# Optimization experiments

Measured on AMD Instinct MI355X. Metric: run time of the kernel, lower is better.

The kernel has to match this reference:

```python
import jax, jax.numpy as jnp
import numpy as np

B, S, D, H = 2, 2048, 1024, 16
DH = D // H  # dim_per_head = 64


def setup_inputs() -> dict:
    key = jax.random.key(0)
    ks = jax.random.split(key, 12)
    scale = 1.0 / np.sqrt(D)
    inp = {
        "key": jax.random.normal(ks[0], (B, S, D), jnp.float32),
        "value": jax.random.normal(ks[1], (B, S, D), jnp.float32),
        "query": jax.random.normal(ks[2], (B, S, D), jnp.float32),
        "mask": jnp.zeros((B, S, S), dtype=bool),
        # nn.Linear weights stored as [out, in]; we keep [in, out] for x @ W
        "Wk": jax.random.normal(ks[3], (D, D), jnp.float32) * scale,
        "bk": jnp.zeros((D,), jnp.float32),
        "Wv": jax.random.normal(ks[4], (D, D), jnp.float32) * scale,
        "bv": jnp.zeros((D,), jnp.float32),
        "Wq": jax.random.normal(ks[5], (D, D), jnp.float32) * scale,
        "bq": jnp.zeros((D,), jnp.float32),
        "Wo": jax.random.normal(ks[6], (D, D), jnp.float32) * scale,
        "bo": jnp.zeros((D,), jnp.float32),
    }
    return inp


def reference(key, value, query, mask, Wk, bk, Wv, bv, Wq, bq, Wo, bo):
    # project and split heads: [B, S, D] -> [B, H, S, DH]
    def shape(x):
        return x.reshape(B, S, H, DH).transpose(0, 2, 1, 3)

    k = shape(key @ Wk + bk)
    v = shape(value @ Wv + bv)
    q = shape(query @ Wq + bq) / jnp.sqrt(jnp.asarray(DH, key.dtype))

    # scores: [B, H, Sq, Sk]
    scores = jnp.einsum("bhqd,bhkd->bhqk", q, k)
    scores = jnp.where(mask[:, None, :, :], jnp.asarray(-1e10, scores.dtype), scores)
    attn = jax.nn.softmax(scores, axis=-1)
    # dropout is identity in eval mode
    context = jnp.einsum("bhqk,bhkd->bhqd", attn, v)
    context = context.transpose(0, 2, 1, 3).reshape(B, S, D)
    output = context @ Wo + bo
    return output, attn
```

## Files before the change

kernel.cpp:

```cpp
#include <hip/hip_runtime.h>

#define B_  2
#define S_  2048
#define D_  1024
#define H_  16

typedef _Float16 h8 __attribute__((ext_vector_type(8)));
typedef _Float16 h4 __attribute__((ext_vector_type(4)));
typedef float f4 __attribute__((ext_vector_type(4)));

static __device__ __forceinline__ f4 mfma16(h8 a, h8 b, f4 c) {
  return __builtin_amdgcn_mfma_f32_16x16x32_f16(a, b, c, 0, 0, 0);
}

static __device__ __forceinline__ void gload16(const void* g, void* l) {
  __builtin_amdgcn_global_load_lds(
      (const __attribute__((address_space(1))) void*)g,
      (__attribute__((address_space(3))) void*)l, 16, 0, 0);
}

struct C3 { const float* in[3]; _Float16* out[3]; };
__global__ __launch_bounds__(256) void cvt3_kernel(C3 c) {
  const float* in = c.in[blockIdx.y];
  _Float16* out = c.out[blockIdx.y];
  const size_t i = ((size_t)blockIdx.x * 256 + threadIdx.x) * 8;
  float4 a = *(const float4*)(in + i);
  float4 b = *(const float4*)(in + i + 4);
  h8 v;
  v[0]=(_Float16)a.x; v[1]=(_Float16)a.y; v[2]=(_Float16)a.z; v[3]=(_Float16)a.w;
  v[4]=(_Float16)b.x; v[5]=(_Float16)b.y; v[6]=(_Float16)b.z; v[7]=(_Float16)b.w;
  *(h8*)(out + i) = v;
}

struct W4 { const float* w[4]; _Float16* wt[4]; };
__global__ __launch_bounds__(256) void wtrans4_kernel(W4 a) {
  const float* W = a.w[blockIdx.z];
  _Float16* WT = a.wt[blockIdx.z];
  __shared__ float tile[64][65];
  const int t = threadIdx.x;
  const int bi = blockIdx.x * 64;
  const int bj = blockIdx.y * 64;
  const int row = t >> 2, c0 = (t & 3) * 16;
  const float* src = W + (size_t)(bi + row) * D_ + bj + c0;
#pragma unroll
  for (int j = 0; j < 4; j++) {
    float4 v = *(const float4*)(src + j * 4);
    tile[row][c0 + j*4 + 0] = v.x; tile[row][c0 + j*4 + 1] = v.y;
    tile[row][c0 + j*4 + 2] = v.z; tile[row][c0 + j*4 + 3] = v.w;
  }
  __syncthreads();
  h8 o0, o1;
#pragma unroll
  for (int j = 0; j < 8; j++) o0[j] = (_Float16)tile[c0 + j][row];
#pragma unroll
  for (int j = 0; j < 8; j++) o1[j] = (_Float16)tile[c0 + 8 + j][row];
  _Float16* dst = WT + (size_t)(bj + row) * D_ + bi + c0;
  *(h8*)(dst)     = o0;
  *(h8*)(dst + 8) = o1;
}

__global__ __launch_bounds__(256) void maskflag_kernel(const unsigned char* __restrict__ mask,
                                                       unsigned char* __restrict__ flags) {
  __shared__ int s;
  const int t = threadIdx.x;
  const int kt = blockIdx.x, qb = blockIdx.y, b = blockIdx.z;
  if (t == 0) s = 0;
  __syncthreads();
  const unsigned char* mp = mask + ((size_t)(b * S_ + qb * 128 + (t >> 1))) * S_
                          + kt * 64 + (t & 1) * 32;
  const uint4* p = (const uint4*)mp;
  uint4 v = p[0], w = p[1];
  unsigned int o = v.x | v.y | v.z | v.w | w.x | w.y | w.z | w.w;
  if (o) s = 1;
  __syncthreads();
  if (t == 0) flags[((size_t)b * 16 + qb) * 32 + kt] = (unsigned char)s;
}

struct GArg { const _Float16* A; const _Float16* BT; const float* bias;
              void* out; float scale; int mode; };
struct G3 { GArg a[3]; };

__global__ __launch_bounds__(256, 3) void gemmp_kernel(G3 G) {
  const GArg g = G.a[blockIdx.z];
  const _Float16* __restrict__ A  = g.A;
  const _Float16* __restrict__ BT = g.BT;
  __shared__ _Float16 Ash[128 * 64];
  __shared__ _Float16 Bsh[128 * 64];
  const int t = threadIdx.x, lane = t & 63, wave = t >> 6;
  const int lrow = lane & 15, lq = lane >> 4;
  const int m0 = blockIdx.x * 128, n0 = blockIdx.y * 128;
  const int wm = wave >> 1, wn = wave & 1;
  f4 acc[4][4];
#pragma unroll
  for (int i = 0; i < 4; i++)
#pragma unroll
    for (int j = 0; j < 4; j++) acc[i][j] = f4{0.f, 0.f, 0.f, 0.f};
  float bb[4];
#pragma unroll
  for (int j = 0; j < 4; j++) bb[j] = g.bias[n0 + wn*64 + j*16 + lrow];

  const int srow = t >> 3;
  const int lch  = (t & 7) ^ (srow & 7);
  const _Float16* asrc = A  + (size_t)(m0 + srow) * D_ + lch * 8;
  const _Float16* bsrc = BT + (size_t)(n0 + srow) * D_ + lch * 8;

  for (int k0 = 0; k0 < D_; k0 += 64) {
#pragma unroll
    for (int rnd = 0; rnd < 4; rnd++)
      gload16(asrc + (size_t)(rnd * 32) * D_ + k0,
              (char*)Ash + rnd * 4096 + wave * 1024);
#pragma unroll
    for (int rnd = 0; rnd < 4; rnd++)
      gload16(bsrc + (size_t)(rnd * 32) * D_ + k0,
              (char*)Bsh + rnd * 4096 + wave * 1024);
    __syncthreads();
#pragma unroll
    for (int kf = 0; kf < 2; kf++) {
      h8 af[4], bf[4];
#pragma unroll
      for (int i = 0; i < 4; i++) {
        int rr = wm*64 + i*16 + lrow;
        int ch = (kf*4 + lq) ^ (rr & 7);
        af[i] = *(h8*)((char*)Ash + rr*128 + ch*16);
      }
#pragma unroll
      for (int j = 0; j < 4; j++) {
        int rr = wn*64 + j*16 + lrow;
        int ch = (kf*4 + lq) ^ (rr & 7);
        bf[j] = *(h8*)((char*)Bsh + rr*128 + ch*16);
      }
#pragma unroll
      for (int i = 0; i < 4; i++)
#pragma unroll
        for (int j = 0; j < 4; j++)
          acc[i][j] = mfma16(af[i], bf[j], acc[i][j]);
    }
    __syncthreads();
  }

  if (g.mode == 0) {
    _Float16* out = (_Float16*)g.out;
#pragma unroll
    for (int i = 0; i < 4; i++) {
      int m = m0 + wm*64 + i*16 + lq*4;
#pragma unroll
      for (int j = 0; j < 4; j++) {
        int n = n0 + wn*64 + j*16 + lrow;
#pragma unroll
        for (int r = 0; r < 4; r++)
          out[(size_t)(m + r) * D_ + n] = (_Float16)((acc[i][j][r] + bb[j]) * g.scale);
      }
    }
  } else if (g.mode == 1) {
    _Float16* out = (_Float16*)g.out;
#pragma unroll
    for (int i = 0; i < 4; i++) {
      int m = m0 + wm*64 + i*16 + lq*4;
      int b = m >> 11, s = m & (S_ - 1);
#pragma unroll
      for (int j = 0; j < 4; j++) {
        int n = n0 + wn*64 + j*16 + lrow;
        int hh = n >> 6, dh = n & 63;
        h4 hv;
#pragma unroll
        for (int r = 0; r < 4; r++) hv[r] = (_Float16)(acc[i][j][r] + bb[j]);
        *(h4*)(out + ((size_t)((b * H_ + hh) * 64 + dh)) * S_ + s) = hv;
      }
    }
  } else {
    float* out = (float*)g.out;
#pragma unroll
    for (int i = 0; i < 4; i++) {
      int m = m0 + wm*64 + i*16 + lq*4;
#pragma unroll
      for (int j = 0; j < 4; j++) {
        int n = n0 + wn*64 + j*16 + lrow;
#pragma unroll
        for (int r = 0; r < 4; r++)
          out[(size_t)(m + r) * D_ + n] = acc[i][j][r] + bb[j];
      }
    }
  }
}

__global__ __launch_bounds__(512, 4) void gemmz_kernel(G3 G) {
  const GArg g = G.a[blockIdx.z];
  const _Float16* __restrict__ A  = g.A;
  const _Float16* __restrict__ BT = g.BT;
  __shared__ _Float16 Ash[128 * 64];
  __shared__ _Float16 Bsh[128 * 64];
  const int t = threadIdx.x, lane = t & 63, wave = t >> 6;
  const int lrow = lane & 15, lq = lane >> 4;
  const int m0 = blockIdx.x * 128, n0 = blockIdx.y * 128;
  const int wm = wave >> 2, wn = wave & 3;
  f4 acc[4][2];
#pragma unroll
  for (int i = 0; i < 4; i++)
#pragma unroll
    for (int j = 0; j < 2; j++) acc[i][j] = f4{0.f, 0.f, 0.f, 0.f};
  float bb[2];
#pragma unroll
  for (int j = 0; j < 2; j++) bb[j] = g.bias[n0 + wn*32 + j*16 + lrow];

  const int srow = t >> 3;
  const int lch  = (t & 7) ^ (srow & 7);
  const _Float16* a0 = A  + (size_t)(m0 + srow)      * D_ + lch * 8;
  const _Float16* a1 = A  + (size_t)(m0 + 64 + srow) * D_ + lch * 8;
  const _Float16* b0 = BT + (size_t)(n0 + srow)      * D_ + lch * 8;
  const _Float16* b1 = BT + (size_t)(n0 + 64 + srow) * D_ + lch * 8;
  char* adst0 = (char*)Ash + wave * 1024;
  char* adst1 = (char*)Ash + 8192 + wave * 1024;
  char* bdst0 = (char*)Bsh + wave * 1024;
  char* bdst1 = (char*)Bsh + 8192 + wave * 1024;

  for (int k0 = 0; k0 < D_; k0 += 64) {
    gload16(a0 + k0, adst0);
    gload16(a1 + k0, adst1);
    gload16(b0 + k0, bdst0);
    gload16(b1 + k0, bdst1);
    __syncthreads();
#pragma unroll
    for (int kf = 0; kf < 2; kf++) {
      h8 af[4], bf[2];
#pragma unroll
      for (int i = 0; i < 4; i++) {
        int rr = wm*64 + i*16 + lrow;
        int ch = (kf*4 + lq) ^ (rr & 7);
        af[i] = *(h8*)((char*)Ash + rr*128 + ch*16);
      }
#pragma unroll
      for (int j = 0; j < 2; j++) {
        int rr = wn*32 + j*16 + lrow;
        int ch = (kf*4 + lq) ^ (rr & 7);
        bf[j] = *(h8*)((char*)Bsh + rr*128 + ch*16);
      }
#pragma unroll
      for (int i = 0; i < 4; i++)
#pragma unroll
        for (int j = 0; j < 2; j++)
          acc[i][j] = mfma16(af[i], bf[j], acc[i][j]);
    }
    __syncthreads();
  }

  if (g.mode == 0) {
    _Float16* out = (_Float16*)g.out;
#pragma unroll
    for (int i = 0; i < 4; i++) {
      int m = m0 + wm*64 + i*16 + lq*4;
#pragma unroll
      for (int j = 0; j < 2; j++) {
        int n = n0 + wn*32 + j*16 + lrow;
#pragma unroll
        for (int r = 0; r < 4; r++)
          out[(size_t)(m + r) * D_ + n] = (_Float16)((acc[i][j][r] + bb[j]) * g.scale);
      }
    }
  } else if (g.mode == 1) {
    _Float16* out = (_Float16*)g.out;
#pragma unroll
    for (int i = 0; i < 4; i++) {
      int m = m0 + wm*64 + i*16 + lq*4;
      int b = m >> 11, s = m & (S_ - 1);
#pragma unroll
      for (int j = 0; j < 2; j++) {
        int n = n0 + wn*32 + j*16 + lrow;
        int hh = n >> 6, dh = n & 63;
        h4 hv;
#pragma unroll
        for (int r = 0; r < 4; r++) hv[r] = (_Float16)(acc[i][j][r] + bb[j]);
        *(h4*)(out + ((size_t)((b * H_ + hh) * 64 + dh)) * S_ + s) = hv;
      }
    }
  } else {
    float* out = (float*)g.out;
#pragma unroll
    for (int i = 0; i < 4; i++) {
      int m = m0 + wm*64 + i*16 + lq*4;
#pragma unroll
      for (int j = 0; j < 2; j++) {
        int n = n0 + wn*32 + j*16 + lrow;
#pragma unroll
        for (int r = 0; r < 4; r++)
          out[(size_t)(m + r) * D_ + n] = acc[i][j][r] + bb[j];
      }
    }
  }
}

__global__ __launch_bounds__(256, 4) void attnF_kernel(
    const _Float16* __restrict__ Qp, const _Float16* __restrict__ Kp,
    const _Float16* __restrict__ VpT, const unsigned char* __restrict__ mask,
    const unsigned char* __restrict__ flags,
    float* __restrict__ attn, _Float16* __restrict__ CtxH)
{
  __shared__ char smem[40960];
  const int t = threadIdx.x, lane = t & 63, wave = t >> 6;
  const int lrow = lane & 15, lq = lane >> 4;
  const int logical = ((blockIdx.x & 7) << 7) + (blockIdx.x >> 3);
  const int bh = logical >> 5, qb = logical & 31;
  const int b = bh >> 4, h = bh & 15;
  const int q0 = qb * 64, qw = q0 + wave * 16;

  h8 qf0, qf1;
  {
    const _Float16* qp = Qp + ((size_t)(b * S_ + qw + lrow)) * D_ + h * 64 + lq * 8;
    qf0 = *(const h8*)qp;
    qf1 = *(const h8*)(qp + 32);
  }

  const int srow = t >> 3, klch = (t & 7) ^ (srow & 7);
  const _Float16* ksrc = Kp + ((size_t)(b * S_ + srow)) * D_ + h * 64 + klch * 8;
  char* kdst = smem + wave * 1024;
  const unsigned char* mflags = flags + ((size_t)(b * 16 + (qb >> 1))) * 32;
  const unsigned char* mrow0 = mask + ((size_t)(b * S_ + qw + lq*4)) * S_ + lrow;

  float lsum[4] = {0.f, 0.f, 0.f, 0.f};
  for (int kt = 0; kt < S_; kt += 256) {
#pragma unroll
    for (int rnd = 0; rnd < 8; rnd++)
      gload16(ksrc + (size_t)(kt + rnd * 32) * D_, kdst + rnd * 4096);
    __syncthreads();
#pragma unroll
    for (int c = 0; c < 16; c++) {
      int kr = c*16 + lrow, sx = kr & 7;
      h8 k0 = *(h8*)(smem + kr*128 + ((lq     ^ sx) << 4));
      h8 k1 = *(h8*)(smem + kr*128 + (((4+lq) ^ sx) << 4));
      f4 a = f4{0.f, 0.f, 0.f, 0.f};
      __builtin_amdgcn_s_setprio(1);
      a = mfma16(qf0, k0, a);
      a = mfma16(qf1, k1, a);
      __builtin_amdgcn_s_setprio(0);
      if (mflags[(kt >> 6) + (c >> 2)]) {
#pragma unroll
        for (int r = 0; r < 4; r++)
          if (mrow0[(size_t)r * S_ + kt + c*16]) a[r] = -1e10f;
      }
#pragma unroll
      for (int r = 0; r < 4; r++) lsum[r] += __expf(fminf(a[r], 75.f));
    }
    __syncthreads();
  }

  float li[4];
#pragma unroll
  for (int r = 0; r < 4; r++) {
    float cs = lsum[r];
#pragma unroll
    for (int d = 1; d < 16; d <<= 1) cs += __shfl_xor(cs, d);
    li[r] = 1.0f / cs;
  }

  char* const Vt = smem + 16384;
  char* const Pt = smem + 32768;
  const int vrow = t >> 4, vlch = (t & 15) ^ (vrow & 15);
  const _Float16* vsrc = VpT + (size_t)bh * 64 * S_ + (size_t)vrow * S_ + vlch * 8;
  char* vdst = Vt + wave * 1024;

  f4 ctx[4];
#pragma unroll
  for (int dt = 0; dt < 4; dt++) ctx[dt] = f4{0.f, 0.f, 0.f, 0.f};

  for (int kt = 0; kt < S_; kt += 128) {
#pragma unroll
    for (int rnd = 0; rnd < 4; rnd++)
      gload16(ksrc + (size_t)(kt + rnd * 32) * D_, kdst + rnd * 4096);
#pragma unroll
    for (int rnd = 0; rnd < 4; rnd++)
      gload16(vsrc + (size_t)(rnd * 16) * S_ + kt, vdst + rnd * 4096);
    __syncthreads();

#pragma unroll
    for (int hh = 0; hh < 2; hh++) {
      const int kbase = kt + hh * 64;
      const bool mf = mflags[kbase >> 6] != 0;
      const int prw = wave*16 + lq*4;
#pragma unroll
      for (int c = 0; c < 4; c++) {
        int kr = hh*64 + c*16 + lrow, sx = kr & 7;
        h8 k0 = *(h8*)(smem + kr*128 + ((lq     ^ sx) << 4));
        h8 k1 = *(h8*)(smem + kr*128 + (((4+lq) ^ sx) << 4));
        f4 a = f4{0.f, 0.f, 0.f, 0.f};
        __builtin_amdgcn_s_setprio(1);
        a = mfma16(qf0, k0, a);
        a = mfma16(qf1, k1, a);
        __builtin_amdgcn_s_setprio(0);
        if (mf) {
#pragma unroll
          for (int r = 0; r < 4; r++)
            if (mrow0[(size_t)r * S_ + kbase + c*16]) a[r] = -1e10f;
        }
        float* ap = attn + ((size_t)bh * S_ + qw + lq*4) * S_ + kbase + c*16 + lrow;
        int eb = c*32 + lrow*2;
#pragma unroll
        for (int r = 0; r < 4; r++) {
          float p = __expf(fminf(a[r], 75.f)) * li[r];
          ap[(size_t)r * S_] = p;
          int rw = prw + r;
          *(_Float16*)(Pt + rw*128 + ((((eb >> 4) ^ (rw & 7))) << 4) + (eb & 15))
              = (_Float16)p;
        }
      }
      {
        int pr2 = wave*16 + lrow, sxp = pr2 & 7;
        h8 pf0 = *(h8*)(Pt + pr2*128 + (((    lq) ^ sxp) << 4));
        h8 pf1 = *(h8*)(Pt + pr2*128 + (((4 + lq) ^ sxp) << 4));
        __builtin_amdgcn_s_setprio(1);
#pragma unroll
        for (int dt = 0; dt < 4; dt++) {
          int vr = dt*16 + lrow, sxv = vr & 15;
          h8 vf0 = *(h8*)(Vt + vr*256 + (((hh*8     + lq) ^ sxv) << 4));
          h8 vf1 = *(h8*)(Vt + vr*256 + (((hh*8 + 4 + lq) ^ sxv) << 4));
          ctx[dt] = mfma16(pf0, vf0, ctx[dt]);
          ctx[dt] = mfma16(pf1, vf1, ctx[dt]);
        }
        __builtin_amdgcn_s_setprio(0);
      }
    }
    __syncthreads();
  }

  _Float16* cp = CtxH + ((size_t)(b * S_ + qw + lq*4)) * D_ + h * 64 + lrow;
#pragma unroll
  for (int dt = 0; dt < 4; dt++)
#pragma unroll
    for (int r = 0; r < 4; r++)
      cp[(size_t)r * D_ + dt*16] = (_Float16)ctx[dt][r];
}

extern "C" void kernel_launch(void* const* d_in, const int* in_sizes, int n_in,
                              void* d_out, int out_size, void* d_ws, size_t ws_size,
                              hipStream_t stream) {
  const float* key   = (const float*)d_in[0];
  const float* value = (const float*)d_in[1];
  const float* query = (const float*)d_in[2];
  const unsigned char* mask = (const unsigned char*)d_in[3];
  const float* Wk = (const float*)d_in[4];
  const float* bk = (const float*)d_in[5];
  const float* Wv = (const float*)d_in[6];
  const float* bv = (const float*)d_in[7];
  const float* Wq = (const float*)d_in[8];
  const float* bq = (const float*)d_in[9];
  const float* Wo = (const float*)d_in[10];
  const float* bo = (const float*)d_in[11];

  char* ws = (char*)d_ws;
  _Float16* WkT  = (_Float16*)(ws + 0);
  _Float16* WvT  = (_Float16*)(ws + (size_t)2  * 1024 * 1024);
  _Float16* WqT  = (_Float16*)(ws + (size_t)4  * 1024 * 1024);
  _Float16* WoT  = (_Float16*)(ws + (size_t)6  * 1024 * 1024);
  _Float16* Qp   = (_Float16*)(ws + (size_t)8  * 1024 * 1024);
  _Float16* Kp   = (_Float16*)(ws + (size_t)16 * 1024 * 1024);
  _Float16* VpT  = (_Float16*)(ws + (size_t)24 * 1024 * 1024);
  _Float16* CtxH = (_Float16*)(ws + (size_t)32 * 1024 * 1024);
  unsigned char* flags = (unsigned char*)(ws + (size_t)40 * 1024 * 1024);

  float* outp = (float*)d_out;
  float* attn = outp + (size_t)B_ * S_ * D_;
  _Float16* qH = (_Float16*)(attn);
  _Float16* kH = (_Float16*)((char*)attn + (size_t)8  * 1024 * 1024);
  _Float16* vH = (_Float16*)((char*)attn + (size_t)16 * 1024 * 1024);

  C3 c{{query, key, value}, {qH, kH, vH}};
  cvt3_kernel<<<dim3(2048, 3), 256, 0, stream>>>(c);

  W4 w{{Wk, Wv, Wq, Wo}, {WkT, WvT, WqT, WoT}};
  wtrans4_kernel<<<dim3(16, 16, 4), 256, 0, stream>>>(w);

  maskflag_kernel<<<dim3(32, 16, 2), 256, 0, stream>>>(mask, flags);

  G3 gp{{{qH, WqT, bq, Qp, 0.125f, 0},
         {kH, WkT, bk, Kp, 1.0f,   0},
         {vH, WvT, bv, VpT, 1.0f,  1}}};
  gemmp_kernel<<<dim3(32, 8, 3), 256, 0, stream>>>(gp);

  attnF_kernel<<<1024, 256, 0, stream>>>(Qp, Kp, VpT, mask, flags, attn, CtxH);

  G3 go{{{CtxH, WoT, bo, outp, 1.0f, 2},
         {nullptr, nullptr, nullptr, nullptr, 0.f, 2},
         {nullptr, nullptr, nullptr, nullptr, 0.f, 2}}};
  gemmz_kernel<<<dim3(32, 8, 1), 512, 0, stream>>>(go);
}
```

Measured before the change: 279.0 us.

## Split softmax-denominator pass by key columns across waves with LDS reduction

In the first pass computing row sums of exp(scores), each wave now handles all 64 query rows of the block but only a quarter of each 256-key tile, instead of its own 16 rows over all keys. Each K fragment read from LDS is reused across four query groups, cutting LDS reads per MFMA. Per-wave partial sums are combined through shared memory with an extra barrier. This raises register use (four Q fragment pairs and a 4x4 accumulator array), which may hurt occupancy under launch bounds of 4 blocks.

```diff
diff --git a/kernel.cpp b/kernel.cpp
--- a/kernel.cpp
+++ b/kernel.cpp
@@ -302,54 +302,81 @@
   const int b = bh >> 4, h = bh & 15;
   const int q0 = qb * 64, qw = q0 + wave * 16;
 
+  const int srow = t >> 3, klch = (t & 7) ^ (srow & 7);
+  const _Float16* ksrc = Kp + ((size_t)(b * S_ + srow)) * D_ + h * 64 + klch * 8;
+  char* kdst = smem + wave * 1024;
+  const unsigned char* mflags = flags + ((size_t)(b * 16 + (qb >> 1))) * 32;
+
+  h8 qfA[4][2];
+#pragma unroll
+  for (int g = 0; g < 4; g++) {
+    const _Float16* qp = Qp + ((size_t)(b * S_ + q0 + g*16 + lrow)) * D_ + h * 64 + lq * 8;
+    qfA[g][0] = *(const h8*)qp;
+    qfA[g][1] = *(const h8*)(qp + 32);
+  }
+  const unsigned char* mA = mask + ((size_t)(b * S_ + q0 + lq*4)) * S_ + lrow;
+
+  float lsum[4][4];
+#pragma unroll
+  for (int g = 0; g < 4; g++)
+#pragma unroll
+    for (int r = 0; r < 4; r++) lsum[g][r] = 0.f;
+
+  for (int kt = 0; kt < S_; kt += 256) {
+#pragma unroll
+    for (int rnd = 0; rnd < 8; rnd++)
+      gload16(ksrc + (size_t)(kt + rnd * 32) * D_, kdst + rnd * 4096);
+    __syncthreads();
+    const bool mf = mflags[(kt >> 6) + wave] != 0;
+#pragma unroll
+    for (int c = 0; c < 4; c++) {
+      int kr = wave*64 + c*16 + lrow, sx = kr & 7;
+      h8 k0 = *(h8*)(smem + kr*128 + ((lq     ^ sx) << 4));
+      h8 k1 = *(h8*)(smem + kr*128 + (((4+lq) ^ sx) << 4));
+#pragma unroll
+      for (int g = 0; g < 4; g++) {
+        f4 a = f4{0.f, 0.f, 0.f, 0.f};
+        __builtin_amdgcn_s_setprio(1);
+        a = mfma16(qfA[g][0], k0, a);
+        a = mfma16(qfA[g][1], k1, a);
+        __builtin_amdgcn_s_setprio(0);
+        if (mf) {
+#pragma unroll
+          for (int r = 0; r < 4; r++)
+            if (mA[(size_t)(g*16 + r) * S_ + kt + wave*64 + c*16]) a[r] = -1e10f;
+        }
+#pragma unroll
+        for (int r = 0; r < 4; r++) lsum[g][r] += __expf(fminf(a[r], 75.f));
+      }
+    }
+    __syncthreads();
+  }
+
+  float* partial = (float*)(smem + 32768);
+#pragma unroll
+  for (int g = 0; g < 4; g++)
+#pragma unroll
+    for (int r = 0; r < 4; r++) {
+      float cs = lsum[g][r];
+#pragma unroll
+      for (int d = 1; d < 16; d <<= 1) cs += __shfl_xor(cs, d);
+      if (lrow == 0) partial[wave*64 + g*16 + lq*4 + r] = cs;
+    }
+  __syncthreads();
+  float li[4];
+#pragma unroll
+  for (int r = 0; r < 4; r++) {
+    int ql = wave*16 + lq*4 + r;
+    li[r] = 1.0f / (partial[ql] + partial[64 + ql] + partial[128 + ql] + partial[192 + ql]);
+  }
+
   h8 qf0, qf1;
   {
     const _Float16* qp = Qp + ((size_t)(b * S_ + qw + lrow)) * D_ + h * 64 + lq * 8;
     qf0 = *(const h8*)qp;
     qf1 = *(const h8*)(qp + 32);
   }
-
-  const int srow = t >> 3, klch = (t & 7) ^ (srow & 7);
-  const _Float16* ksrc = Kp + ((size_t)(b * S_ + srow)) * D_ + h * 64 + klch * 8;
-  char* kdst = smem + wave * 1024;
-  const unsigned char* mflags = flags + ((size_t)(b * 16 + (qb >> 1))) * 32;
   const unsigned char* mrow0 = mask + ((size_t)(b * S_ + qw + lq*4)) * S_ + lrow;
-
-  float lsum[4] = {0.f, 0.f, 0.f, 0.f};
-  for (int kt = 0; kt < S_; kt += 256) {
-#pragma unroll
-    for (int rnd = 0; rnd < 8; rnd++)
-      gload16(ksrc + (size_t)(kt + rnd * 32) * D_, kdst + rnd * 4096);
-    __syncthreads();
-#pragma unroll
-    for (int c = 0; c < 16; c++) {
-      int kr = c*16 + lrow, sx = kr & 7;
-      h8 k0 = *(h8*)(smem + kr*128 + ((lq     ^ sx) << 4));
-      h8 k1 = *(h8*)(smem + kr*128 + (((4+lq) ^ sx) << 4));
-      f4 a = f4{0.f, 0.f, 0.f, 0.f};
-      __builtin_amdgcn_s_setprio(1);
-      a = mfma16(qf0, k0, a);
-      a = mfma16(qf1, k1, a);
-      __builtin_amdgcn_s_setprio(0);
-      if (mflags[(kt >> 6) + (c >> 2)]) {
-#pragma unroll
-        for (int r = 0; r < 4; r++)
-          if (mrow0[(size_t)r * S_ + kt + c*16]) a[r] = -1e10f;
-      }
-#pragma unroll
-      for (int r = 0; r < 4; r++) lsum[r] += __expf(fminf(a[r], 75.f));
-    }
-    __syncthreads();
-  }
-
-  float li[4];
-#pragma unroll
-  for (int r = 0; r < 4; r++) {
-    float cs = lsum[r];
-#pragma unroll
-    for (int d = 1; d < 16; d <<= 1) cs += __shfl_xor(cs, d);
-    li[r] = 1.0f / cs;
-  }
 
   char* const Vt = smem + 16384;
   char* const Pt = smem + 32768;
```

Result: slower. 297.5 us (+6.6%).

## Load K and V fragments directly from global memory instead of staging through LDS

Applied to the files above, without the earlier changes.

Removes the shared-memory staging of K and V tiles, which used global_load_lds and block-wide barriers, from both attention passes. Each wave now reads its MFMA operands straight from global memory, relying on L1/L2 for reuse across the four waves. This drops the __syncthreads calls and shrinks LDS to just the P tile, which may allow higher occupancy. The cost is repeated global traffic from every wave, plus load latency that is no longer hidden behind the bulk LDS copies.

```diff
diff --git a/kernel.cpp b/kernel.cpp
--- a/kernel.cpp
+++ b/kernel.cpp
@@ -294,7 +294,7 @@
     const unsigned char* __restrict__ flags,
     float* __restrict__ attn, _Float16* __restrict__ CtxH)
 {
-  __shared__ char smem[40960];
+  __shared__ char Pt[8192];
   const int t = threadIdx.x, lane = t & 63, wave = t >> 6;
   const int lrow = lane & 15, lq = lane >> 4;
   const int logical = ((blockIdx.x & 7) << 7) + (blockIdx.x >> 3);
@@ -309,115 +309,90 @@
     qf1 = *(const h8*)(qp + 32);
   }
 
-  const int srow = t >> 3, klch = (t & 7) ^ (srow & 7);
-  const _Float16* ksrc = Kp + ((size_t)(b * S_ + srow)) * D_ + h * 64 + klch * 8;
-  char* kdst = smem + wave * 1024;
+  const _Float16* kb = Kp + (size_t)(b * S_) * D_ + h * 64;
+  const _Float16* vb = VpT + (size_t)bh * 64 * S_;
   const unsigned char* mflags = flags + ((size_t)(b * 16 + (qb >> 1))) * 32;
   const unsigned char* mrow0 = mask + ((size_t)(b * S_ + qw + lq*4)) * S_ + lrow;
 
   float lsum[4] = {0.f, 0.f, 0.f, 0.f};
-  for (int kt = 0; kt < S_; kt += 256) {
-#pragma unroll
-    for (int rnd = 0; rnd < 8; rnd++)
-      gload16(ksrc + (size_t)(kt + rnd * 32) * D_, kdst + rnd * 4096);
-    __syncthreads();
-#pragma unroll
-    for (int c = 0; c < 16; c++) {
-      int kr = c*16 + lrow, sx = kr & 7;
-      h8 k0 = *(h8*)(smem + kr*128 + ((lq     ^ sx) << 4));
-      h8 k1 = *(h8*)(smem + kr*128 + (((4+lq) ^ sx) << 4));
+#pragma unroll 4
+  for (int kk = 0; kk < S_ / 16; kk++) {
+    const _Float16* kp = kb + (size_t)(kk*16 + lrow) * D_;
+    h8 k0 = *(const h8*)(kp + lq*8);
+    h8 k1 = *(const h8*)(kp + 32 + lq*8);
+    f4 a = f4{0.f, 0.f, 0.f, 0.f};
+    __builtin_amdgcn_s_setprio(1);
+    a = mfma16(qf0, k0, a);
+    a = mfma16(qf1, k1, a);
+    __builtin_amdgcn_s_setprio(0);
+    if (mflags[kk >> 2]) {
+#pragma unroll
+      for (int r = 0; r < 4; r++)
+        if (mrow0[(size_t)r * S_ + kk*16]) a[r] = -1e10f;
+    }
+#pragma unroll
+    for (int r = 0; r < 4; r++) lsum[r] += __expf(fminf(a[r], 75.f));
+  }
+
+  float li[4];
+#pragma unroll
+  for (int r = 0; r < 4; r++) {
+    float cs = lsum[r];
+#pragma unroll
+    for (int d = 1; d < 16; d <<= 1) cs += __shfl_xor(cs, d);
+    li[r] = 1.0f / cs;
+  }
+
+  f4 ctx[4];
+#pragma unroll
+  for (int dt = 0; dt < 4; dt++) ctx[dt] = f4{0.f, 0.f, 0.f, 0.f};
+
+  const int prw = wave*16 + lq*4;
+  const int pr2 = wave*16 + lrow, sxp = pr2 & 7;
+
+  for (int hb = 0; hb < S_ / 64; hb++) {
+    const int kbase = hb * 64;
+    const bool mf = mflags[hb] != 0;
+#pragma unroll
+    for (int c = 0; c < 4; c++) {
+      const _Float16* kp = kb + (size_t)(kbase + c*16 + lrow) * D_;
+      h8 k0 = *(const h8*)(kp + lq*8);
+      h8 k1 = *(const h8*)(kp + 32 + lq*8);
       f4 a = f4{0.f, 0.f, 0.f, 0.f};
       __builtin_amdgcn_s_setprio(1);
       a = mfma16(qf0, k0, a);
       a = mfma16(qf1, k1, a);
       __builtin_amdgcn_s_setprio(0);
-      if (mflags[(kt >> 6) + (c >> 2)]) {
+      if (mf) {
 #pragma unroll
         for (int r = 0; r < 4; r++)
-          if (mrow0[(size_t)r * S_ + kt + c*16]) a[r] = -1e10f;
-      }
-#pragma unroll
-      for (int r = 0; r < 4; r++) lsum[r] += __expf(fminf(a[r], 75.f));
-    }
-    __syncthreads();
-  }
-
-  float li[4];
-#pragma unroll
-  for (int r = 0; r < 4; r++) {
-    float cs = lsum[r];
-#pragma unroll
-    for (int d = 1; d < 16; d <<= 1) cs += __shfl_xor(cs, d);
-    li[r] = 1.0f / cs;
-  }
-
-  char* const Vt = smem + 16384;
-  char* const Pt = smem + 32768;
-  const int vrow = t >> 4, vlch = (t & 15) ^ (vrow & 15);
-  const _Float16* vsrc = VpT + (size_t)bh * 64 * S_ + (size_t)vrow * S_ + vlch * 8;
-  char* vdst = Vt + wave * 1024;
-
-  f4 ctx[4];
-#pragma unroll
-  for (int dt = 0; dt < 4; dt++) ctx[dt] = f4{0.f, 0.f, 0.f, 0.f};
-
-  for (int kt = 0; kt < S_; kt += 128) {
-#pragma unroll
-    for (int rnd = 0; rnd < 4; rnd++)
-      gload16(ksrc + (size_t)(kt + rnd * 32) * D_, kdst + rnd * 4096);
-#pragma unroll
-    for (int rnd = 0; rnd < 4; rnd++)
-      gload16(vsrc + (size_t)(rnd * 16) * S_ + kt, vdst + rnd * 4096);
-    __syncthreads();
-
-#pragma unroll
-    for (int hh = 0; hh < 2; hh++) {
-      const int kbase = kt + hh * 64;
-      const bool mf = mflags[kbase >> 6] != 0;
-      const int prw = wave*16 + lq*4;
-#pragma unroll
-      for (int c = 0; c < 4; c++) {
-        int kr = hh*64 + c*16 + lrow, sx = kr & 7;
-        h8 k0 = *(h8*)(smem + kr*128 + ((lq     ^ sx) << 4));
-        h8 k1 = *(h8*)(smem + kr*128 + (((4+lq) ^ sx) << 4));
-        f4 a = f4{0.f, 0.f, 0.f, 0.f};
-        __builtin_amdgcn_s_setprio(1);
-        a = mfma16(qf0, k0, a);
-        a = mfma16(qf1, k1, a);
-        __builtin_amdgcn_s_setprio(0);
-        if (mf) {
-#pragma unroll
-          for (int r = 0; r < 4; r++)
-            if (mrow0[(size_t)r * S_ + kbase + c*16]) a[r] = -1e10f;
-        }
-        float* ap = attn + ((size_t)bh * S_ + qw + lq*4) * S_ + kbase + c*16 + lrow;
-        int eb = c*32 + lrow*2;
-#pragma unroll
-        for (int r = 0; r < 4; r++) {
-          float p = __expf(fminf(a[r], 75.f)) * li[r];
-          ap[(size_t)r * S_] = p;
-          int rw = prw + r;
-          *(_Float16*)(Pt + rw*128 + ((((eb >> 4) ^ (rw & 7))) << 4) + (eb & 15))
-              = (_Float16)p;
-        }
-      }
-      {
-        int pr2 = wave*16 + lrow, sxp = pr2 & 7;
-        h8 pf0 = *(h8*)(Pt + pr2*128 + (((    lq) ^ sxp) << 4));
-        h8 pf1 = *(h8*)(Pt + pr2*128 + (((4 + lq) ^ sxp) << 4));
-        __builtin_amdgcn_s_setprio(1);
-#pragma unroll
-        for (int dt = 0; dt < 4; dt++) {
-          int vr = dt*16 + lrow, sxv = vr & 15;
-          h8 vf0 = *(h8*)(Vt + vr*256 + (((hh*8     + lq) ^ sxv) << 4));
-          h8 vf1 = *(h8*)(Vt + vr*256 + (((hh*8 + 4 + lq) ^ sxv) << 4));
-          ctx[dt] = mfma16(pf0, vf0, ctx[dt]);
-          ctx[dt] = mfma16(pf1, vf1, ctx[dt]);
-        }
-        __builtin_amdgcn_s_setprio(0);
-      }
-    }
-    __syncthreads();
+          if (mrow0[(size_t)r * S_ + kbase + c*16]) a[r] = -1e10f;
+      }
+      float* ap = attn + ((size_t)bh * S_ + qw + lq*4) * S_ + kbase + c*16 + lrow;
+      int eb = c*32 + lrow*2;
+#pragma unroll
+      for (int r = 0; r < 4; r++) {
+        float p = __expf(fminf(a[r], 75.f)) * li[r];
+        ap[(size_t)r * S_] = p;
+        int rw = prw + r;
+        *(_Float16*)(Pt + rw*128 + ((((eb >> 4) ^ (rw & 7))) << 4) + (eb & 15))
+            = (_Float16)p;
+      }
+    }
+    {
+      h8 pf0 = *(h8*)(Pt + pr2*128 + (((    lq) ^ sxp) << 4));
+      h8 pf1 = *(h8*)(Pt + pr2*128 + (((4 + lq) ^ sxp) << 4));
+      __builtin_amdgcn_s_setprio(1);
+#pragma unroll
+      for (int dt = 0; dt < 4; dt++) {
+        const _Float16* vp = vb + (size_t)(dt*16 + lrow) * S_ + kbase;
+        h8 vf0 = *(const h8*)(vp + lq*8);
+        h8 vf1 = *(const h8*)(vp + 32 + lq*8);
+        ctx[dt] = mfma16(pf0, vf0, ctx[dt]);
+        ctx[dt] = mfma16(pf1, vf1, ctx[dt]);
+      }
+      __builtin_amdgcn_s_setprio(0);
+    }
   }
 
   _Float16* cp = CtxH + ((size_t)(b * S_ + qw + lq*4)) * D_ + h * 64 + lrow;
```

Measured after the change: 533.1 us. 91.1% more time.
